# Kernel tuning notes

Hardware: AMD Instinct MI355X
Metric: run time of the kernel (lower is better)

Reference implementation:

```python
import jax, jax.numpy as jnp
import numpy as np

LN_EPS = 1e-5
TOP_K = 2


def _layernorm(x, g, b):
    mu = jnp.mean(x, axis=-1, keepdims=True)
    var = jnp.var(x, axis=-1, keepdims=True)
    return (x - mu) * jax.lax.rsqrt(var + LN_EPS) * g + b


def _moe_layer(x, ln_g, ln_b, Wr, br, We, be):
    # x: [B,T,H]; Wr: [H,E]; We: [E,H,H]; be: [E,H]
    E = Wr.shape[-1]
    z = _layernorm(x, ln_g, ln_b)
    logits = jnp.einsum('bth,he->bte', z, Wr) + br
    probs = jax.nn.softmax(logits, axis=-1)
    # top-k masking + renormalization (top_k < num_experts)
    topv, topi = jax.lax.top_k(probs, TOP_K)                      # [B,T,K]
    mask = (jax.nn.one_hot(topi, E, dtype=probs.dtype) * topv[..., None]).sum(-2)  # [B,T,E]
    w = mask / jnp.clip(mask.sum(-1, keepdims=True), 1e-8)
    # dense all-expert compute (faithful to torch.stack over experts), masked combine
    outs = jnp.einsum('bth,ehd->bted', z, We) + be                # [B,T,E,H]
    mixed = jnp.einsum('bte,bted->btd', w, outs)
    return x + mixed


def setup_inputs() -> dict:
    key = jax.random.key(0)
    B, T, H, E, L = 4, 2048, 3072, 4, 2
    ks = jax.random.split(key, 4)
    s = 1.0 / np.sqrt(H)
    x = jax.random.normal(ks[0], (B, T, H), dtype=jnp.float32)
    ln_g = jnp.ones((L, H), jnp.float32)
    ln_b = jnp.zeros((L, H), jnp.float32)
    Wr = jax.random.normal(ks[1], (L, H, E), jnp.float32) * s
    br = jnp.zeros((L, E), jnp.float32)
    We = jax.random.normal(ks[2], (L, E, H, H), jnp.float32) * s
    be = jnp.zeros((L, E, H), jnp.float32)
    return {"x": x, "ln_g": ln_g, "ln_b": ln_b, "Wr": Wr, "br": br, "We": We, "be": be}


def reference(x, ln_g, ln_b, Wr, br, We, be):
    L = ln_g.shape[0]
    for i in range(L):  # fixed small layer count
        x = _moe_layer(x, ln_g[i], ln_b[i], Wr[i], br[i], We[i], be[i])
    return x
```

## Files before the change

kernel.cpp:

```cpp
#include <hip/hip_runtime.h>
#include <hip/hip_bf16.h>
#include <stdint.h>

#define H 3072
#define EXPERTS 4
#define MTOK 8192
#define LN_EPS 1e-5f
#define FLAG_CAP 1024
#define TAU 0.03f
#define NT_MAX 70
#define KSPLIT 2

#define BM 128
#define BN 128
#define BK 32
#define BKG 64

typedef __bf16 bf16;
typedef __bf16 bf16x8 __attribute__((ext_vector_type(8)));
typedef __bf16 bf16x4 __attribute__((ext_vector_type(4)));
typedef float  f32x4  __attribute__((ext_vector_type(4)));

typedef const __attribute__((address_space(1))) unsigned char* gas1p;
typedef __attribute__((address_space(3))) unsigned char* las3p;

__device__ __forceinline__ void gload_lds16(const void* g, void* l) {
    __builtin_amdgcn_global_load_lds((gas1p)g, (las3p)l, 16, 0, 0);
}

__device__ __forceinline__ int pair_a(int b) { return b < 3 ? 0 : (b < 5 ? 1 : 2); }
__device__ __forceinline__ int pair_b(int b) { return b < 3 ? b + 1 : (b < 5 ? b - 1 : 3); }

template <int WLO>
__global__ __launch_bounds__(256) void we_transpose(const float* __restrict__ We,
                                                    bf16* __restrict__ Wt_hi,
                                                    bf16* __restrict__ Wt_lo) {
    __shared__ float tile[64][65];
    const int e  = blockIdx.z;
    const int k0 = blockIdx.y * 64;
    const int n0 = blockIdx.x * 64;
    const int tid = threadIdx.x;

    const float* src = We + ((size_t)e * H + k0) * H + n0;
    const int kl = tid >> 4;
    const int nl = (tid & 15) * 4;
#pragma unroll
    for (int it = 0; it < 4; ++it) {
        float4 v = *(const float4*)(src + (size_t)(kl + it * 16) * H + nl);
        tile[kl + it * 16][nl + 0] = v.x;
        tile[kl + it * 16][nl + 1] = v.y;
        tile[kl + it * 16][nl + 2] = v.z;
        tile[kl + it * 16][nl + 3] = v.w;
    }
    __syncthreads();
    const size_t dbase = ((size_t)e * H + n0) * H + k0;
    const int nl2 = tid >> 4;
    const int kl2 = (tid & 15) * 4;
#pragma unroll
    for (int it = 0; it < 4; ++it) {
        bf16x4 oh, ol;
#pragma unroll
        for (int j = 0; j < 4; ++j) {
            float v = tile[kl2 + j][nl2 + it * 16];
            bf16 hi = (bf16)v;
            oh[j] = hi;
            ol[j] = (bf16)(v - (float)hi);
        }
        const size_t doff = dbase + (size_t)(nl2 + it * 16) * H + kl2;
        *(bf16x4*)(Wt_hi + doff) = oh;
        if (WLO) *(bf16x4*)(Wt_lo + doff) = ol;
    }
}

template <int MODE>
__global__ __launch_bounds__(256) void ln_router_k(const float* __restrict__ xin,
                                                   const float* __restrict__ gamma,
                                                   const float* __restrict__ beta,
                                                   const float* __restrict__ Wr,
                                                   const float* __restrict__ br,
                                                   bf16* __restrict__ z,
                                                   float* __restrict__ wout,
                                                   int* __restrict__ bkt,
                                                   int* __restrict__ bcount,
                                                   int* __restrict__ flags) {
    __shared__ float red[4][4];
    __shared__ float bc[2];

    const int t    = blockIdx.x;
    const int tid  = threadIdx.x;
    const int wid  = tid >> 6;
    const int lane = tid & 63;
    const float* xrow = xin + (size_t)t * H;

    float4 xv[3];
    float s = 0.f;
#pragma unroll
    for (int c = 0; c < 3; ++c) {
        xv[c] = *(const float4*)(xrow + (c * 256 + tid) * 4);
        s += xv[c].x + xv[c].y + xv[c].z + xv[c].w;
    }
#pragma unroll
    for (int off = 32; off; off >>= 1) s += __shfl_down(s, off);
    if (lane == 0) red[wid][0] = s;
    __syncthreads();
    if (tid == 0) bc[0] = (red[0][0] + red[1][0] + red[2][0] + red[3][0]) * (1.f / (float)H);
    __syncthreads();
    const float mu = bc[0];

    float d = 0.f;
#pragma unroll
    for (int c = 0; c < 3; ++c) {
        float dx;
        dx = xv[c].x - mu; d += dx * dx;
        dx = xv[c].y - mu; d += dx * dx;
        dx = xv[c].z - mu; d += dx * dx;
        dx = xv[c].w - mu; d += dx * dx;
    }
#pragma unroll
    for (int off = 32; off; off >>= 1) d += __shfl_down(d, off);
    if (lane == 0) red[wid][1] = d;
    __syncthreads();
    if (tid == 0) {
        float var = (red[0][1] + red[1][1] + red[2][1] + red[3][1]) * (1.f / (float)H);
        bc[1] = 1.f / sqrtf(var + LN_EPS);
    }
    __syncthreads();
    const float rs = bc[1];

    float l0 = 0.f, l1 = 0.f, l2 = 0.f, l3 = 0.f;
    bf16* zrow = z + (size_t)t * H;
#pragma unroll
    for (int c = 0; c < 3; ++c) {
        const int i0 = (c * 256 + tid) * 4;
        float4 gv = *(const float4*)(gamma + i0);
        float4 bv = *(const float4*)(beta + i0);
        float zz[4];
        zz[0] = (xv[c].x - mu) * rs * gv.x + bv.x;
        zz[1] = (xv[c].y - mu) * rs * gv.y + bv.y;
        zz[2] = (xv[c].z - mu) * rs * gv.z + bv.z;
        zz[3] = (xv[c].w - mu) * rs * gv.w + bv.w;
        if (MODE == 0) {
            bf16x4 zb = { (bf16)zz[0], (bf16)zz[1], (bf16)zz[2], (bf16)zz[3] };
            *(bf16x4*)(zrow + i0) = zb;
        }
#pragma unroll
        for (int j = 0; j < 4; ++j) {
            float4 wr = *(const float4*)(Wr + (size_t)(i0 + j) * 4);
            l0 += zz[j] * wr.x; l1 += zz[j] * wr.y;
            l2 += zz[j] * wr.z; l3 += zz[j] * wr.w;
        }
    }
    __syncthreads();
#pragma unroll
    for (int off = 32; off; off >>= 1) {
        l0 += __shfl_down(l0, off);
        l1 += __shfl_down(l1, off);
        l2 += __shfl_down(l2, off);
        l3 += __shfl_down(l3, off);
    }
    if (lane == 0) { red[wid][0] = l0; red[wid][1] = l1; red[wid][2] = l2; red[wid][3] = l3; }
    __syncthreads();
    if (tid == 0) {
        float lf[4];
#pragma unroll
        for (int e = 0; e < 4; ++e)
            lf[e] = red[0][e] + red[1][e] + red[2][e] + red[3][e] + br[e];
        if (MODE == 0) {
            float mx = fmaxf(fmaxf(lf[0], lf[1]), fmaxf(lf[2], lf[3]));
            float p[4]; float ps = 0.f;
#pragma unroll
            for (int e = 0; e < 4; ++e) { p[e] = expf(lf[e] - mx); ps += p[e]; }
#pragma unroll
            for (int e = 0; e < 4; ++e) p[e] /= ps;
            int i1 = 0; float v1 = p[0];
#pragma unroll
            for (int e = 1; e < 4; ++e) if (p[e] > v1) { v1 = p[e]; i1 = e; }
            int i2 = -1; float v2 = -1.f;
#pragma unroll
            for (int e = 0; e < 4; ++e) if (e != i1 && p[e] > v2) { v2 = p[e]; i2 = e; }
            const float den = fmaxf(v1 + v2, 1e-8f);
            float w4[4] = {0.f, 0.f, 0.f, 0.f};
            w4[i1] = v1 / den;
            w4[i2] = v2 / den;
            *(float4*)(wout + (size_t)t * 4) = make_float4(w4[0], w4[1], w4[2], w4[3]);
            const int lo = min(i1, i2), hi = max(i1, i2);
            const int b = (lo == 0) ? hi - 1 : (lo == 1 ? hi + 1 : 5);
            bkt[t] = b;
            atomicAdd(&bcount[b], 1);
        } else {
            float a = lf[0], b = lf[1], c = lf[2], dd = lf[3], t1;
#define SW_(p,q) if (p < q) { t1 = p; p = q; q = t1; }
            SW_(a, b) SW_(c, dd) SW_(a, c) SW_(b, dd) SW_(b, c)
#undef SW_
            if (b - c < TAU) {
                int idx = atomicAdd(flags, 1);
                if (idx < FLAG_CAP) flags[1 + idx] = t;
            }
        }
    }
}

__global__ void zero_flags(int* flags) { if (threadIdx.x == 0) flags[0] = 0; }
__global__ void zero12(int* bcount) { if (threadIdx.x < 12) bcount[threadIdx.x] = 0; }

__global__ __launch_bounds__(256) void bucket_scan(const int* __restrict__ bcount,
                                                   int* __restrict__ off_g,
                                                   int* __restrict__ tile_bkt,
                                                   int* __restrict__ tile_end,
                                                   int* __restrict__ tokslot) {
    for (int i = threadIdx.x; i < NT_MAX * BM; i += 256) tokslot[i] = 0;
    if (threadIdx.x == 0) {
        int off = 0, tile = 0;
        for (int b = 0; b < 6; ++b) {
            off_g[b] = off;
            const int c = bcount[b];
            const int ntb = (c + BM - 1) / BM;
            for (int k = 0; k < ntb; ++k) { tile_bkt[tile] = b; tile_end[tile] = off + c; ++tile; }
            off += ntb * BM;
        }
        for (; tile < NT_MAX; ++tile) { tile_bkt[tile] = -1; tile_end[tile] = 0; }
    }
}

__global__ __launch_bounds__(256) void scatter(const int* __restrict__ bkt,
                                               const int* __restrict__ off_g,
                                               int* __restrict__ cursor,
                                               int* __restrict__ tokslot,
                                               int* __restrict__ slot_of) {
    const int t = blockIdx.x * 256 + threadIdx.x;
    if (t >= MTOK) return;
    const int b = bkt[t];
    const int slot = off_g[b] + atomicAdd(&cursor[b], 1);
    tokslot[slot] = t;
    slot_of[t] = slot;
}

__global__ __launch_bounds__(384) void scatter_scale(const bf16* __restrict__ z,
                                                     const float* __restrict__ wb,
                                                     const int* __restrict__ bkt,
                                                     const int* __restrict__ slot_of,
                                                     bf16* __restrict__ zA,
                                                     bf16* __restrict__ zB) {
    const int t = blockIdx.x;
    const int b = bkt[t];
    const float wa = wb[(size_t)t * 4 + pair_a(b)];
    const float wv = wb[(size_t)t * 4 + pair_b(b)];
    const size_t slot = (size_t)slot_of[t];
    const int i0 = threadIdx.x * 8;
    const bf16x8 v = *(const bf16x8*)(z + (size_t)t * H + i0);
    bf16x8 ra, rb;
#pragma unroll
    for (int j = 0; j < 8; ++j) {
        const float f = (float)v[j];
        ra[j] = (bf16)(f * wa);
        rb[j] = (bf16)(f * wv);
    }
    *(bf16x8*)(zA + slot * H + i0) = ra;
    *(bf16x8*)(zB + slot * H + i0) = rb;
}

__global__ __launch_bounds__(256) void zfill(const float* __restrict__ x,
                                             const float* __restrict__ gamma,
                                             const float* __restrict__ beta,
                                             const int* __restrict__ flags,
                                             const float* __restrict__ wb,
                                             bf16* __restrict__ zc_hi,
                                             bf16* __restrict__ zc_lo,
                                             float* __restrict__ wfo) {
    __shared__ float red[4][2];
    __shared__ float bc[2];
    const int i = blockIdx.x;
    int count = flags[0]; if (count > FLAG_CAP) count = FLAG_CAP;
    if (i >= count) return;
    const int t = flags[1 + i];
    const int tid = threadIdx.x, wid = tid >> 6, lane = tid & 63;
    const float* xrow = x + (size_t)t * H;

    float4 xv[3]; float s = 0.f;
#pragma unroll
    for (int c = 0; c < 3; ++c) {
        xv[c] = *(const float4*)(xrow + (c * 256 + tid) * 4);
        s += xv[c].x + xv[c].y + xv[c].z + xv[c].w;
    }
#pragma unroll
    for (int off = 32; off; off >>= 1) s += __shfl_down(s, off);
    if (lane == 0) red[wid][0] = s;
    __syncthreads();
    if (tid == 0) bc[0] = (red[0][0] + red[1][0] + red[2][0] + red[3][0]) * (1.f / (float)H);
    __syncthreads();
    const float mu = bc[0];
    float d = 0.f;
#pragma unroll
    for (int c = 0; c < 3; ++c) {
        float dx;
        dx = xv[c].x - mu; d += dx * dx;
        dx = xv[c].y - mu; d += dx * dx;
        dx = xv[c].z - mu; d += dx * dx;
        dx = xv[c].w - mu; d += dx * dx;
    }
#pragma unroll
    for (int off = 32; off; off >>= 1) d += __shfl_down(d, off);
    if (lane == 0) red[wid][1] = d;
    __syncthreads();
    if (tid == 0) bc[1] = 1.f / sqrtf((red[0][1] + red[1][1] + red[2][1] + red[3][1]) * (1.f / (float)H) + LN_EPS);
    __syncthreads();
    const float rs = bc[1];

    bf16* zh = zc_hi + (size_t)i * H;
    bf16* zl = zc_lo + (size_t)i * H;
#pragma unroll
    for (int c = 0; c < 3; ++c) {
        const int i0 = (c * 256 + tid) * 4;
        float4 gv = *(const float4*)(gamma + i0);
        float4 bv = *(const float4*)(beta + i0);
        float vv[4];
        vv[0] = (xv[c].x - mu) * rs * gv.x + bv.x;
        vv[1] = (xv[c].y - mu) * rs * gv.y + bv.y;
        vv[2] = (xv[c].z - mu) * rs * gv.z + bv.z;
        vv[3] = (xv[c].w - mu) * rs * gv.w + bv.w;
        bf16x4 oh, ol;
#pragma unroll
        for (int j = 0; j < 4; ++j) {
            bf16 hi = (bf16)vv[j];
            oh[j] = hi;
            ol[j] = (bf16)(vv[j] - (float)hi);
        }
        *(bf16x4*)(zh + i0) = oh;
        *(bf16x4*)(zl + i0) = ol;
    }
    if (tid == 0) *(float4*)(wfo + (size_t)i * 4) = *(const float4*)(wb + (size_t)t * 4);
}

__global__ __launch_bounds__(256) void refine_mfma(const bf16* __restrict__ zc_hi,
                                                   const bf16* __restrict__ zc_lo,
                                                   const bf16* __restrict__ Wt_hi,
                                                   const bf16* __restrict__ Wt_lo,
                                                   const float* __restrict__ wf,
                                                   const int* __restrict__ flags,
                                                   float* __restrict__ partial) {
    int count = flags[0]; if (count > FLAG_CAP) count = FLAG_CAP;
    const int tileM = blockIdx.y * BM;
    if (tileM >= count) return;
    const int ez = blockIdx.z;
    const int e  = ez >> 1;
    const int ks = ez & 1;
    const int kbeg = ks * (H / KSPLIT / BK);
    const int kend = kbeg + H / KSPLIT / BK;

    __shared__ __align__(16) bf16 Ah[2][BM * BK];
    __shared__ __align__(16) bf16 Al[2][BM * BK];
    __shared__ __align__(16) bf16 Bh[2][BN * BK];
    __shared__ __align__(16) bf16 Bl[2][BN * BK];
    __shared__ float wlds[BM];

    const int tid  = threadIdx.x;
    const int wid  = tid >> 6;
    const int lane = tid & 63;
    const int wm   = wid >> 1;
    const int wn   = wid & 1;
    const int tileN = blockIdx.x * BN;

    if (tid < 128) wlds[tid] = wf[(size_t)(tileM + tid) * 4 + e];

    const int srow   = lane >> 2;
    const int schunk = (((lane & 3) ^ ((lane >> 3) & 3)) * 8);
    const int lrow   = lane & 15;
    const int rchunk = (((lane >> 4) ^ ((lane >> 1) & 3)) * 8);
    const int r0   = wm * 64 + (lane >> 4) * 4;
    const int c0   = tileN + wn * 64 + (lane & 15);

    const bf16* Ahb = zc_hi;
    const bf16* Alb = zc_lo;
    const bf16* Bhb = Wt_hi + ((size_t)e * H + tileN) * H;
    const bf16* Blb = Wt_lo + ((size_t)e * H + tileN) * H;

#define RSTAGE(buf, kk0)                                                              \
    _Pragma("unroll")                                                                 \
    for (int i_ = 0; i_ < 2; ++i_) {                                                  \
        const int rr_ = wid * 32 + i_ * 16;                                           \
        gload_lds16(Ahb + (size_t)(tileM + rr_ + srow) * H + (kk0) + schunk,          \
                    &Ah[buf][(size_t)rr_ * BK]);                                      \
        gload_lds16(Alb + (size_t)(tileM + rr_ + srow) * H + (kk0) + schunk,          \
                    &Al[buf][(size_t)rr_ * BK]);                                      \
        gload_lds16(Bhb + (size_t)(rr_ + srow) * H + (kk0) + schunk,                  \
                    &Bh[buf][(size_t)rr_ * BK]);                                      \
        gload_lds16(Blb + (size_t)(rr_ + srow) * H + (kk0) + schunk,                  \
                    &Bl[buf][(size_t)rr_ * BK]);                                      \
    }

    f32x4 acc[4][4];
#pragma unroll
    for (int m = 0; m < 4; ++m)
#pragma unroll
        for (int n = 0; n < 4; ++n)
            acc[m][n] = (f32x4){0.f, 0.f, 0.f, 0.f};

    RSTAGE(0, kbeg * BK)
    __syncthreads();

    int cur = 0;
    for (int kk = kbeg; kk < kend; ++kk) {
        if (kk + 1 < kend) { RSTAGE(cur ^ 1, (kk + 1) * BK) }

        bf16x8 ah[4], al[4], bh[4], bl[4];
#pragma unroll
        for (int m = 0; m < 4; ++m) {
            ah[m] = *(const bf16x8*)&Ah[cur][(wm * 64 + m * 16 + lrow) * BK + rchunk];
            al[m] = *(const bf16x8*)&Al[cur][(wm * 64 + m * 16 + lrow) * BK + rchunk];
        }
#pragma unroll
        for (int n = 0; n < 4; ++n) {
            bh[n] = *(const bf16x8*)&Bh[cur][(wn * 64 + n * 16 + lrow) * BK + rchunk];
            bl[n] = *(const bf16x8*)&Bl[cur][(wn * 64 + n * 16 + lrow) * BK + rchunk];
        }
#pragma unroll
        for (int m = 0; m < 4; ++m)
#pragma unroll
            for (int n = 0; n < 4; ++n) {
                acc[m][n] = __builtin_amdgcn_mfma_f32_16x16x32_bf16(al[m], bh[n], acc[m][n], 0, 0, 0);
                acc[m][n] = __builtin_amdgcn_mfma_f32_16x16x32_bf16(ah[m], bl[n], acc[m][n], 0, 0, 0);
                acc[m][n] = __builtin_amdgcn_mfma_f32_16x16x32_bf16(ah[m], bh[n], acc[m][n], 0, 0, 0);
            }
        __syncthreads();
        cur ^= 1;
    }
#undef RSTAGE

#pragma unroll
    for (int m = 0; m < 4; ++m) {
#pragma unroll
        for (int r = 0; r < 4; ++r) {
            const int tl = r0 + m * 16 + r;
            const int g = tileM + tl;
            if (g < count) {
                const float w = wlds[tl];
                float* prow = partial + ((size_t)ez * FLAG_CAP + g) * H;
#pragma unroll
                for (int n = 0; n < 4; ++n)
                    prow[c0 + n * 16] = w * acc[m][n][r];
            }
        }
    }
}

__global__ __launch_bounds__(256) void refine_combine(const float* __restrict__ partial,
                                                      const float* __restrict__ x,
                                                      const float* __restrict__ wf,
                                                      const float* __restrict__ be,
                                                      const int* __restrict__ flags,
                                                      float* __restrict__ out) {
    int count = flags[0]; if (count > FLAG_CAP) count = FLAG_CAP;
    const int i = blockIdx.x;
    if (i >= count) return;
    const int t = flags[1 + i];
    const int tid = threadIdx.x;
    const float4 wq = *(const float4*)(wf + (size_t)i * 4);
#pragma unroll
    for (int c = 0; c < 3; ++c) {
        const int col = (c * 256 + tid) * 4;
        float4 s = *(const float4*)(x + (size_t)t * H + col);
#pragma unroll
        for (int ez = 0; ez < EXPERTS * KSPLIT; ++ez) {
            float4 p = *(const float4*)(partial + ((size_t)ez * FLAG_CAP + i) * H + col);
            s.x += p.x; s.y += p.y; s.z += p.z; s.w += p.w;
        }
        const float4 b0 = *(const float4*)(be + 0 * H + col);
        const float4 b1 = *(const float4*)(be + 1 * H + col);
        const float4 b2 = *(const float4*)(be + 2 * H + col);
        const float4 b3 = *(const float4*)(be + 3 * H + col);
        s.x += wq.x * b0.x + wq.y * b1.x + wq.z * b2.x + wq.w * b3.x;
        s.y += wq.x * b0.y + wq.y * b1.y + wq.z * b2.y + wq.w * b3.y;
        s.z += wq.x * b0.z + wq.y * b1.z + wq.z * b2.z + wq.w * b3.z;
        s.w += wq.x * b0.w + wq.y * b1.w + wq.z * b2.w + wq.w * b3.w;
        *(float4*)(out + (size_t)t * H + col) = s;
    }
}

__global__ __launch_bounds__(256, 4) void moe_gemm_b(const bf16* __restrict__ zA,
                                                     const bf16* __restrict__ zB,
                                                     const bf16* __restrict__ Wt,
                                                     const int* __restrict__ tokslot,
                                                     const float* __restrict__ wbuf,
                                                     const int* __restrict__ tile_bkt,
                                                     const int* __restrict__ tile_end,
                                                     const float* __restrict__ xin,
                                                     const float* __restrict__ be,
                                                     float* __restrict__ out) {
    const int tile = blockIdx.y;
    const int b = tile_bkt[tile];
    if (b < 0) return;
    const int ea = pair_a(b);
    const int eb = pair_b(b);
    const int endSlot = tile_end[tile];

    __shared__ __align__(16) bf16 As[BM * BKG];
    __shared__ __align__(16) bf16 Bs[BN * BKG];
    __shared__ __align__(16) float wlds[BM * 4];
    __shared__ int tlds[BM];

    const int tid  = threadIdx.x;
    const int wid  = tid >> 6;
    const int lane = tid & 63;
    const int wm   = wid >> 1;
    const int wn   = wid & 1;
    const int tileM = tile * BM;
    const int tileN = blockIdx.x * BN;

    if (tid < 128) {
        const int tk = tokslot[tileM + tid];
        tlds[tid] = tk;
        *(float4*)&wlds[tid * 4] = *(const float4*)(wbuf + (size_t)tk * 4);
    }

    const int srow   = lane >> 3;
    const int schunk = (((lane & 7) ^ ((lane >> 3) & 7)) * 8);
    const int lrow   = lane & 15;
    const int rx     = lane >> 4;
    const int r0   = wm * 64 + (lane >> 4) * 4;
    const int c0   = tileN + wn * 64 + (lane & 15);

    f32x4 acc[4][4];
#pragma unroll
    for (int m = 0; m < 4; ++m)
#pragma unroll
        for (int n = 0; n < 4; ++n)
            acc[m][n] = (f32x4){0.f, 0.f, 0.f, 0.f};

    for (int ph = 0; ph < 2; ++ph) {
        const bf16* Asrc = ph ? zB : zA;
        const int ex = ph ? eb : ea;
        const bf16* Bbase = Wt + ((size_t)ex * H + tileN) * H;

        for (int k0 = 0; k0 < H; k0 += BKG) {
            __syncthreads();
#pragma unroll
            for (int i = 0; i < 4; ++i) {
                const int rr = wid * 32 + i * 8;
                gload_lds16(Asrc + (size_t)(tileM + rr + srow) * H + k0 + schunk,
                            As + (size_t)rr * BKG);
                gload_lds16(Bbase + (size_t)(rr + srow) * H + k0 + schunk,
                            Bs + (size_t)rr * BKG);
            }
            __syncthreads();

#pragma unroll
            for (int ks = 0; ks < 2; ++ks) {
                bf16x8 a[4], bfr[4];
#pragma unroll
                for (int m = 0; m < 4; ++m) {
                    const int row = wm * 64 + m * 16 + lrow;
                    const int ch = ((ks * 4 + rx) ^ (lrow & 7)) * 8;
                    a[m] = *(const bf16x8*)&As[row * BKG + ch];
                }
#pragma unroll
                for (int n = 0; n < 4; ++n) {
                    const int row = wn * 64 + n * 16 + lrow;
                    const int ch = ((ks * 4 + rx) ^ (lrow & 7)) * 8;
                    bfr[n] = *(const bf16x8*)&Bs[row * BKG + ch];
                }
#pragma unroll
                for (int m = 0; m < 4; ++m)
#pragma unroll
                    for (int n = 0; n < 4; ++n)
                        acc[m][n] = __builtin_amdgcn_mfma_f32_16x16x32_bf16(a[m], bfr[n], acc[m][n], 0, 0, 0);
            }
        }
    }

    float bev[4][4];
#pragma unroll
    for (int n = 0; n < 4; ++n)
#pragma unroll
        for (int e = 0; e < 4; ++e)
            bev[n][e] = be[(size_t)e * H + c0 + n * 16];

#pragma unroll
    for (int m = 0; m < 4; ++m) {
#pragma unroll
        for (int r = 0; r < 4; ++r) {
            const int tl = r0 + m * 16 + r;
            const int slotg = tileM + tl;
            if (slotg < endSlot) {
                const size_t t = (size_t)tlds[tl];
                const float4 wq = *(const float4*)&wlds[tl * 4];
                const float* xr = xin + t * H;
                float* orow = out + t * H;
#pragma unroll
                for (int n = 0; n < 4; ++n) {
                    const int col = c0 + n * 16;
                    const float bias = wq.x * bev[n][0] + wq.y * bev[n][1] +
                                       wq.z * bev[n][2] + wq.w * bev[n][3];
                    orow[col] = xr[col] + acc[m][n][r] + bias;
                }
            }
        }
    }
}

extern "C" void kernel_launch(void* const* d_in, const int* in_sizes, int n_in,
                              void* d_out, int out_size, void* d_ws, size_t ws_size,
                              hipStream_t stream) {
    (void)in_sizes; (void)n_in; (void)out_size; (void)ws_size;

    const float* x    = (const float*)d_in[0];
    const float* ln_g = (const float*)d_in[1];
    const float* ln_b = (const float*)d_in[2];
    const float* Wr   = (const float*)d_in[3];
    const float* br   = (const float*)d_in[4];
    const float* We   = (const float*)d_in[5];
    const float* be   = (const float*)d_in[6];
    float* out = (float*)d_out;

    uint8_t* ws = (uint8_t*)d_ws;
    const size_t zBytes   = (size_t)MTOK * H * 2;
    const size_t wtBytes  = (size_t)EXPERTS * H * H * 2;
    const size_t wbBytes  = (size_t)MTOK * 4 * 4;
    const size_t zcBytes  = (size_t)FLAG_CAP * H * 2;
    const size_t wfBytes  = (size_t)(FLAG_CAP + 128) * 4 * 4;
    const size_t flgBytes = 8192;
    const size_t zsBytes  = (size_t)NT_MAX * BM * H * 2;

    bf16*  z    = (bf16*)ws;                                       ws += zBytes;
    bf16*  WtH  = (bf16*)ws;                                       ws += wtBytes;
    bf16*  WtL  = (bf16*)ws;                                       ws += wtBytes;
    float* wb   = (float*)ws;                                      ws += wbBytes;
    bf16*  zcH  = (bf16*)ws;                                       ws += zcBytes;
    bf16*  zcL  = (bf16*)ws;                                       ws += zcBytes;
    float* wf   = (float*)ws;                                      ws += wfBytes;
    int*   flg  = (int*)ws;                                        ws += flgBytes;
    bf16*  zA   = (bf16*)ws;                                       ws += zsBytes;
    bf16*  zB   = (bf16*)ws;                                       ws += zsBytes;
    int*   bkt  = (int*)ws;                                        ws += (size_t)MTOK * 4;
    int*   slot_of = (int*)ws;                                     ws += (size_t)MTOK * 4;
    int*   tokslot = (int*)ws;                                     ws += (size_t)NT_MAX * BM * 4;
    int*   bcount  = (int*)ws;                                     ws += 256;
    int*   off_g   = (int*)ws;                                     ws += 256;
    int*   tile_bkt = (int*)ws;                                    ws += 1024;
    int*   tile_end = (int*)ws;                                    ws += 1024;
    int*   cursor = bcount + 6;
    float* partial = (float*)zA;

    const dim3 gemm_grid(H / BN, NT_MAX);

    we_transpose<1><<<dim3(H / 64, H / 64, EXPERTS), 256, 0, stream>>>(We, WtH, WtL);
    zero12<<<1, 64, 0, stream>>>(bcount);
    ln_router_k<0><<<dim3(MTOK), 256, 0, stream>>>(x, ln_g, ln_b, Wr, br, z, wb, bkt, bcount, flg);
    bucket_scan<<<1, 256, 0, stream>>>(bcount, off_g, tile_bkt, tile_end, tokslot);
    scatter<<<dim3(MTOK / 256), 256, 0, stream>>>(bkt, off_g, cursor, tokslot, slot_of);
    scatter_scale<<<dim3(MTOK), 384, 0, stream>>>(z, wb, bkt, slot_of, zA, zB);
    moe_gemm_b<<<gemm_grid, 256, 0, stream>>>(zA, zB, WtH, tokslot, wb, tile_bkt, tile_end, x, be, out);

    zero_flags<<<1, 64, 0, stream>>>(flg);
    ln_router_k<1><<<dim3(MTOK), 256, 0, stream>>>(out, ln_g + H, ln_b + H,
                                                   Wr + (size_t)H * EXPERTS, br + EXPERTS,
                                                   z, wb, bkt, bcount, flg);
    zfill<<<dim3(FLAG_CAP), 256, 0, stream>>>(x, ln_g, ln_b, flg, wb, zcH, zcL, wf);
    refine_mfma<<<dim3(H / BN, FLAG_CAP / BM, EXPERTS * KSPLIT), 256, 0, stream>>>(
        zcH, zcL, WtH, WtL, wf, flg, partial);
    refine_combine<<<dim3(FLAG_CAP), 256, 0, stream>>>(partial, x, wf, be, flg, out);

    we_transpose<0><<<dim3(H / 64, H / 64, EXPERTS), 256, 0, stream>>>(
        We + (size_t)EXPERTS * H * H, WtH, WtL);
    zero12<<<1, 64, 0, stream>>>(bcount);
    ln_router_k<0><<<dim3(MTOK), 256, 0, stream>>>(out, ln_g + H, ln_b + H,
                                                   Wr + (size_t)H * EXPERTS, br + EXPERTS,
                                                   z, wb, bkt, bcount, flg);
    bucket_scan<<<1, 256, 0, stream>>>(bcount, off_g, tile_bkt, tile_end, tokslot);
    scatter<<<dim3(MTOK / 256), 256, 0, stream>>>(bkt, off_g, cursor, tokslot, slot_of);
    scatter_scale<<<dim3(MTOK), 384, 0, stream>>>(z, wb, bkt, slot_of, zA, zB);
    moe_gemm_b<<<gemm_grid, 256, 0, stream>>>(zA, zB, WtH, tokslot, wb, tile_bkt, tile_end, out,
                                              be + (size_t)EXPERTS * H, out);
}
```

Baseline: 1.343 ms.

## Widen transpose stores, fuse scatter into scale, shrink refine M tile

The weight transpose now writes 8-wide bf16 vectors instead of 4-wide, so fewer and larger global stores are issued. The separate scatter kernel is merged into scatter_scale: one thread per block takes the atomic slot and shares it through LDS. This removes a launch and the slot_of buffer. The refine MFMA kernel's M tile drops from 128 to 64 rows, so fewer padded rows are computed when the flagged-token count is small and the grid gets more blocks, at the cost of less B-operand reuse per block.

```diff
diff --git a/kernel.cpp b/kernel.cpp
--- a/kernel.cpp
+++ b/kernel.cpp
@@ -15,6 +15,7 @@
 #define BN 128
 #define BK 32
 #define BKG 64
+#define RBM 64
 
 typedef __bf16 bf16;
 typedef __bf16 bf16x8 __attribute__((ext_vector_type(8)));
@@ -54,21 +55,22 @@
     }
     __syncthreads();
     const size_t dbase = ((size_t)e * H + n0) * H + k0;
-    const int nl2 = tid >> 4;
-    const int kl2 = (tid & 15) * 4;
-#pragma unroll
-    for (int it = 0; it < 4; ++it) {
-        bf16x4 oh, ol;
-#pragma unroll
-        for (int j = 0; j < 4; ++j) {
-            float v = tile[kl2 + j][nl2 + it * 16];
+    const int nl2 = tid >> 3;
+    const int kl2 = (tid & 7) * 8;
+#pragma unroll
+    for (int it = 0; it < 2; ++it) {
+        const int row = nl2 + it * 32;
+        bf16x8 oh, ol;
+#pragma unroll
+        for (int j = 0; j < 8; ++j) {
+            float v = tile[kl2 + j][row];
             bf16 hi = (bf16)v;
             oh[j] = hi;
             ol[j] = (bf16)(v - (float)hi);
         }
-        const size_t doff = dbase + (size_t)(nl2 + it * 16) * H + kl2;
-        *(bf16x4*)(Wt_hi + doff) = oh;
-        if (WLO) *(bf16x4*)(Wt_lo + doff) = ol;
+        const size_t doff = dbase + (size_t)row * H + kl2;
+        *(bf16x8*)(Wt_hi + doff) = oh;
+        if (WLO) *(bf16x8*)(Wt_lo + doff) = ol;
     }
 }
 
@@ -222,30 +224,24 @@
     }
 }
 
-__global__ __launch_bounds__(256) void scatter(const int* __restrict__ bkt,
-                                               const int* __restrict__ off_g,
-                                               int* __restrict__ cursor,
-                                               int* __restrict__ tokslot,
-                                               int* __restrict__ slot_of) {
-    const int t = blockIdx.x * 256 + threadIdx.x;
-    if (t >= MTOK) return;
-    const int b = bkt[t];
-    const int slot = off_g[b] + atomicAdd(&cursor[b], 1);
-    tokslot[slot] = t;
-    slot_of[t] = slot;
-}
-
 __global__ __launch_bounds__(384) void scatter_scale(const bf16* __restrict__ z,
                                                      const float* __restrict__ wb,
                                                      const int* __restrict__ bkt,
-                                                     const int* __restrict__ slot_of,
+                                                     const int* __restrict__ off_g,
+                                                     int* __restrict__ cursor,
+                                                     int* __restrict__ tokslot,
                                                      bf16* __restrict__ zA,
                                                      bf16* __restrict__ zB) {
+    __shared__ int sslot;
     const int t = blockIdx.x;
     const int b = bkt[t];
+    if (threadIdx.x == 0) {
+        const int s = off_g[b] + atomicAdd(&cursor[b], 1);
+        sslot = s;
+        tokslot[s] = t;
+    }
     const float wa = wb[(size_t)t * 4 + pair_a(b)];
     const float wv = wb[(size_t)t * 4 + pair_b(b)];
-    const size_t slot = (size_t)slot_of[t];
     const int i0 = threadIdx.x * 8;
     const bf16x8 v = *(const bf16x8*)(z + (size_t)t * H + i0);
     bf16x8 ra, rb;
@@ -255,6 +251,8 @@
         ra[j] = (bf16)(f * wa);
         rb[j] = (bf16)(f * wv);
     }
+    __syncthreads();
+    const size_t slot = (size_t)sslot;
     *(bf16x8*)(zA + slot * H + i0) = ra;
     *(bf16x8*)(zB + slot * H + i0) = rb;
 }
@@ -339,7 +337,7 @@
                                                    const int* __restrict__ flags,
                                                    float* __restrict__ partial) {
     int count = flags[0]; if (count > FLAG_CAP) count = FLAG_CAP;
-    const int tileM = blockIdx.y * BM;
+    const int tileM = blockIdx.y * RBM;
     if (tileM >= count) return;
     const int ez = blockIdx.z;
     const int e  = ez >> 1;
@@ -347,11 +345,11 @@
     const int kbeg = ks * (H / KSPLIT / BK);
     const int kend = kbeg + H / KSPLIT / BK;
 
-    __shared__ __align__(16) bf16 Ah[2][BM * BK];
-    __shared__ __align__(16) bf16 Al[2][BM * BK];
+    __shared__ __align__(16) bf16 Ah[2][RBM * BK];
+    __shared__ __align__(16) bf16 Al[2][RBM * BK];
     __shared__ __align__(16) bf16 Bh[2][BN * BK];
     __shared__ __align__(16) bf16 Bl[2][BN * BK];
-    __shared__ float wlds[BM];
+    __shared__ float wlds[RBM];
 
     const int tid  = threadIdx.x;
     const int wid  = tid >> 6;
@@ -360,13 +358,13 @@
     const int wn   = wid & 1;
     const int tileN = blockIdx.x * BN;
 
-    if (tid < 128) wlds[tid] = wf[(size_t)(tileM + tid) * 4 + e];
+    if (tid < RBM) wlds[tid] = wf[(size_t)(tileM + tid) * 4 + e];
 
     const int srow   = lane >> 2;
     const int schunk = (((lane & 3) ^ ((lane >> 3) & 3)) * 8);
     const int lrow   = lane & 15;
     const int rchunk = (((lane >> 4) ^ ((lane >> 1) & 3)) * 8);
-    const int r0   = wm * 64 + (lane >> 4) * 4;
+    const int r0   = wm * 32 + (lane >> 4) * 4;
     const int c0   = tileN + wn * 64 + (lane & 15);
 
     const bf16* Ahb = zc_hi;
@@ -375,22 +373,25 @@
     const bf16* Blb = Wt_lo + ((size_t)e * H + tileN) * H;
 
 #define RSTAGE(buf, kk0)                                                              \
-    _Pragma("unroll")                                                                 \
-    for (int i_ = 0; i_ < 2; ++i_) {                                                  \
-        const int rr_ = wid * 32 + i_ * 16;                                           \
-        gload_lds16(Ahb + (size_t)(tileM + rr_ + srow) * H + (kk0) + schunk,          \
-                    &Ah[buf][(size_t)rr_ * BK]);                                      \
-        gload_lds16(Alb + (size_t)(tileM + rr_ + srow) * H + (kk0) + schunk,          \
-                    &Al[buf][(size_t)rr_ * BK]);                                      \
-        gload_lds16(Bhb + (size_t)(rr_ + srow) * H + (kk0) + schunk,                  \
-                    &Bh[buf][(size_t)rr_ * BK]);                                      \
-        gload_lds16(Blb + (size_t)(rr_ + srow) * H + (kk0) + schunk,                  \
-                    &Bl[buf][(size_t)rr_ * BK]);                                      \
-    }
-
-    f32x4 acc[4][4];
-#pragma unroll
-    for (int m = 0; m < 4; ++m)
+    {                                                                                 \
+        const int rrA = wid * 16;                                                     \
+        gload_lds16(Ahb + (size_t)(tileM + rrA + srow) * H + (kk0) + schunk,          \
+                    &Ah[buf][(size_t)rrA * BK]);                                      \
+        gload_lds16(Alb + (size_t)(tileM + rrA + srow) * H + (kk0) + schunk,          \
+                    &Al[buf][(size_t)rrA * BK]);                                      \
+        _Pragma("unroll")                                                             \
+        for (int i_ = 0; i_ < 2; ++i_) {                                              \
+            const int rr_ = wid * 32 + i_ * 16;                                       \
+            gload_lds16(Bhb + (size_t)(rr_ + srow) * H + (kk0) + schunk,              \
+                        &Bh[buf][(size_t)rr_ * BK]);                                  \
+            gload_lds16(Blb + (size_t)(rr_ + srow) * H + (kk0) + schunk,              \
+                        &Bl[buf][(size_t)rr_ * BK]);                                  \
+        }                                                                             \
+    }
+
+    f32x4 acc[2][4];
+#pragma unroll
+    for (int m = 0; m < 2; ++m)
 #pragma unroll
         for (int n = 0; n < 4; ++n)
             acc[m][n] = (f32x4){0.f, 0.f, 0.f, 0.f};
@@ -402,11 +403,11 @@
     for (int kk = kbeg; kk < kend; ++kk) {
         if (kk + 1 < kend) { RSTAGE(cur ^ 1, (kk + 1) * BK) }
 
-        bf16x8 ah[4], al[4], bh[4], bl[4];
-#pragma unroll
-        for (int m = 0; m < 4; ++m) {
-            ah[m] = *(const bf16x8*)&Ah[cur][(wm * 64 + m * 16 + lrow) * BK + rchunk];
-            al[m] = *(const bf16x8*)&Al[cur][(wm * 64 + m * 16 + lrow) * BK + rchunk];
+        bf16x8 ah[2], al[2], bh[4], bl[4];
+#pragma unroll
+        for (int m = 0; m < 2; ++m) {
+            ah[m] = *(const bf16x8*)&Ah[cur][(wm * 32 + m * 16 + lrow) * BK + rchunk];
+            al[m] = *(const bf16x8*)&Al[cur][(wm * 32 + m * 16 + lrow) * BK + rchunk];
         }
 #pragma unroll
         for (int n = 0; n < 4; ++n) {
@@ -414,7 +415,7 @@
             bl[n] = *(const bf16x8*)&Bl[cur][(wn * 64 + n * 16 + lrow) * BK + rchunk];
         }
 #pragma unroll
-        for (int m = 0; m < 4; ++m)
+        for (int m = 0; m < 2; ++m)
 #pragma unroll
             for (int n = 0; n < 4; ++n) {
                 acc[m][n] = __builtin_amdgcn_mfma_f32_16x16x32_bf16(al[m], bh[n], acc[m][n], 0, 0, 0);
@@ -427,7 +428,7 @@
 #undef RSTAGE
 
 #pragma unroll
-    for (int m = 0; m < 4; ++m) {
+    for (int m = 0; m < 2; ++m) {
 #pragma unroll
         for (int r = 0; r < 4; ++r) {
             const int tl = r0 + m * 16 + r;
@@ -631,7 +632,6 @@
     bf16*  zA   = (bf16*)ws;                                       ws += zsBytes;
     bf16*  zB   = (bf16*)ws;                                       ws += zsBytes;
     int*   bkt  = (int*)ws;                                        ws += (size_t)MTOK * 4;
-    int*   slot_of = (int*)ws;                                     ws += (size_t)MTOK * 4;
     int*   tokslot = (int*)ws;                                     ws += (size_t)NT_MAX * BM * 4;
     int*   bcount  = (int*)ws;                                     ws += 256;
     int*   off_g   = (int*)ws;                                     ws += 256;
@@ -646,8 +646,7 @@
     zero12<<<1, 64, 0, stream>>>(bcount);
     ln_router_k<0><<<dim3(MTOK), 256, 0, stream>>>(x, ln_g, ln_b, Wr, br, z, wb, bkt, bcount, flg);
     bucket_scan<<<1, 256, 0, stream>>>(bcount, off_g, tile_bkt, tile_end, tokslot);
-    scatter<<<dim3(MTOK / 256), 256, 0, stream>>>(bkt, off_g, cursor, tokslot, slot_of);
-    scatter_scale<<<dim3(MTOK), 384, 0, stream>>>(z, wb, bkt, slot_of, zA, zB);
+    scatter_scale<<<dim3(MTOK), 384, 0, stream>>>(z, wb, bkt, off_g, cursor, tokslot, zA, zB);
     moe_gemm_b<<<gemm_grid, 256, 0, stream>>>(zA, zB, WtH, tokslot, wb, tile_bkt, tile_end, x, be, out);
 
     zero_flags<<<1, 64, 0, stream>>>(flg);
@@ -655,7 +654,7 @@
                                                    Wr + (size_t)H * EXPERTS, br + EXPERTS,
                                                    z, wb, bkt, bcount, flg);
     zfill<<<dim3(FLAG_CAP), 256, 0, stream>>>(x, ln_g, ln_b, flg, wb, zcH, zcL, wf);
-    refine_mfma<<<dim3(H / BN, FLAG_CAP / BM, EXPERTS * KSPLIT), 256, 0, stream>>>(
+    refine_mfma<<<dim3(H / BN, FLAG_CAP / RBM, EXPERTS * KSPLIT), 256, 0, stream>>>(
         zcH, zcL, WtH, WtL, wf, flg, partial);
     refine_combine<<<dim3(FLAG_CAP), 256, 0, stream>>>(partial, x, wf, be, flg, out);
 
@@ -666,8 +665,7 @@
                                                    Wr + (size_t)H * EXPERTS, br + EXPERTS,
                                                    z, wb, bkt, bcount, flg);
     bucket_scan<<<1, 256, 0, stream>>>(bcount, off_g, tile_bkt, tile_end, tokslot);
-    scatter<<<dim3(MTOK / 256), 256, 0, stream>>>(bkt, off_g, cursor, tokslot, slot_of);
-    scatter_scale<<<dim3(MTOK), 384, 0, stream>>>(z, wb, bkt, slot_of, zA, zB);
+    scatter_scale<<<dim3(MTOK), 384, 0, stream>>>(z, wb, bkt, off_g, cursor, tokslot, zA, zB);
     moe_gemm_b<<<gemm_grid, 256, 0, stream>>>(zA, zB, WtH, tokslot, wb, tile_bkt, tile_end, out,
                                               be + (size_t)EXPERTS * H, out);
 }
```

After: 1.393 ms. +3.7%, slower.
